# Optimization experiments

Hardware: AMD Instinct MI355X
Metric: run time of the kernel (lower is better)

## Reference

```python
import jax, jax.numpy as jnp
import numpy as np

B, HW, NTGT, C = 2, 4096, 4096, 512
H, KNN = 8, 32
DH = C // H
SCALE = DH ** -0.5


def setup_inputs() -> dict:
    key = jax.random.key(0)
    ks = jax.random.split(key, 12)
    s = 1.0 / np.sqrt(C)
    return {
        "src": jax.random.normal(ks[0], (B, HW, C), jnp.float32),
        "tgt": jax.random.normal(ks[1], (B, NTGT, C), jnp.float32),
        "indices": jax.random.randint(ks[2], (B, HW, KNN), 0, NTGT, jnp.int64),
        "weights": jax.random.normal(ks[3], (B, HW, KNN), jnp.float32),
        "Wq": jax.random.normal(ks[4], (C, C), jnp.float32) * s,
        "bq": jnp.zeros((C,), jnp.float32),
        "Wk": jax.random.normal(ks[5], (C, C), jnp.float32) * s,
        "bk": jnp.zeros((C,), jnp.float32),
        "Wv": jax.random.normal(ks[6], (C, C), jnp.float32) * s,
        "bv": jnp.zeros((C,), jnp.float32),
        "Wo": jax.random.normal(ks[7], (C, C), jnp.float32) * s,
        "bo": jnp.zeros((C,), jnp.float32),
    }


def reference(src, tgt, indices, weights, Wq, bq, Wk, bk, Wv, bv, Wo, bo):
    b, hw, c = src.shape
    # projections -> (b, H, seq, dh)
    q = (src @ Wq + bq).reshape(b, hw, H, DH).transpose(0, 2, 1, 3)
    k = (tgt @ Wk + bk).reshape(b, -1, H, DH).transpose(0, 2, 1, 3)
    v = (tgt @ Wv + bv).reshape(b, -1, H, DH).transpose(0, 2, 1, 3)
    # gather epipolar neighbors: per batch, kb[:, idx] -> (H, hw, KNN, dh)
    gather = jax.vmap(lambda xb, ib: xb[:, ib])
    k_g = gather(k, indices)  # (b, H, hw, KNN, dh)
    v_g = gather(v, indices)  # (b, H, hw, KNN, dh)
    logits = jnp.einsum("bhqd,bhqkd->bhqk", q, k_g) * SCALE
    logits = logits + weights[:, None]  # broadcast over heads
    attn = jax.nn.softmax(logits, axis=-1)
    out = jnp.einsum("bhqk,bhqkd->bhqd", attn, v_g)
    out = out.transpose(0, 2, 1, 3).reshape(b, hw, c)
    return out @ Wo + bo
```

## Files before the change

kernel.cpp:

```cpp
#include <hip/hip_runtime.h>
#include <hip/hip_bf16.h>
#include <stdint.h>
#include <type_traits>

#define B_    2
#define HW_   4096
#define NTGT_ 4096
#define C_    512
#define H_    8
#define KNN_  32
#define DH_   64
#define M_    (B_ * HW_)

typedef unsigned short ushort_t;
typedef __bf16 bf16x8 __attribute__((ext_vector_type(8)));
typedef float floatx4 __attribute__((ext_vector_type(4)));

__device__ __forceinline__ float b2f(ushort_t u) {
    union { uint32_t i; float f; } x;
    x.i = ((uint32_t)u) << 16;
    return x.f;
}
__device__ __forceinline__ ushort_t f2b(float f) {
    union { float f; uint32_t i; } x;
    x.f = f;
    uint32_t r = x.i + 0x7fffu + ((x.i >> 16) & 1u);
    return (ushort_t)(r >> 16);
}
__device__ __forceinline__ uint32_t pk2(float x, float y) {
    union { __hip_bfloat162 h2; uint32_t u; } c;
    c.h2 = __float22bfloat162_rn(make_float2(x, y));
    return c.u;
}
__device__ __forceinline__ uint4 pack8(const float4& a, const float4& b) {
    return make_uint4(pk2(a.x, a.y), pk2(a.z, a.w), pk2(b.x, b.y), pk2(b.z, b.w));
}

__global__ __launch_bounds__(256) void transpose_inplace4_f32(
    float* W0, float* W1, float* W2, float* W3) {
    __shared__ float ta[32][33];
    __shared__ float tb[32][33];

    float* W = (blockIdx.y == 0) ? W0 : (blockIdx.y == 1) ? W1
               : (blockIdx.y == 2) ? W2 : W3;

    int p = blockIdx.x;
    int i = 0, acc = 0;
    while (acc + (16 - i) <= p) { acc += 16 - i; ++i; }
    const int j = i + (p - acc);

    const int t = threadIdx.x;
    const int r = t >> 3;
    const int c0 = (t & 7) * 4;

    {
        float4 d = *(const float4*)&W[(size_t)(i * 32 + r) * 512 + j * 32 + c0];
        ta[r][c0 + 0] = d.x; ta[r][c0 + 1] = d.y;
        ta[r][c0 + 2] = d.z; ta[r][c0 + 3] = d.w;
    }
    if (i != j) {
        float4 d = *(const float4*)&W[(size_t)(j * 32 + r) * 512 + i * 32 + c0];
        tb[r][c0 + 0] = d.x; tb[r][c0 + 1] = d.y;
        tb[r][c0 + 2] = d.z; tb[r][c0 + 3] = d.w;
    }
    __syncthreads();

    *(float4*)&W[(size_t)(j * 32 + r) * 512 + i * 32 + c0] =
        make_float4(ta[c0 + 0][r], ta[c0 + 1][r], ta[c0 + 2][r], ta[c0 + 3][r]);
    if (i != j)
        *(float4*)&W[(size_t)(i * 32 + r) * 512 + j * 32 + c0] =
            make_float4(tb[c0 + 0][r], tb[c0 + 1][r], tb[c0 + 2][r], tb[c0 + 3][r]);
}

template <typename AT, typename OT>
__device__ __forceinline__ void gemm_body(const AT* __restrict__ A,
                                          const float* __restrict__ Wt,
                                          const float* __restrict__ bias,
                                          OT* __restrict__ O,
                                          int bm, int bn) {
    __shared__ ushort_t As[128][40];
    __shared__ ushort_t Bs[64][40];

    const int t = threadIdx.x;
    const int ar = t >> 1;
    const int ak = (t & 1) * 16;
    const int br = t >> 2;
    const int bk = (t & 3) * 8;

    const int lane = t & 63;
    const int wv = t >> 6;
    const int wr = (wv >> 1) * 64;
    const int wc = (wv & 1) * 32;
    const int r16 = lane & 15;
    const int quad = lane >> 4;

    floatx4 acc[4][2] = {};

    for (int kt = 0; kt < 512; kt += 32) {
        uint4 av0, av1, bv0;
        if constexpr (std::is_same<AT, float>::value) {
            const float* p = &A[(size_t)(bm + ar) * 512 + kt + ak];
            av0 = pack8(*(const float4*)p, *(const float4*)(p + 4));
            av1 = pack8(*(const float4*)(p + 8), *(const float4*)(p + 12));
        } else {
            const ushort_t* p = &A[(size_t)(bm + ar) * 512 + kt + ak];
            av0 = *(const uint4*)p;
            av1 = *(const uint4*)(p + 8);
        }
        {
            const float* p = &Wt[(size_t)(bn + br) * 512 + kt + bk];
            bv0 = pack8(*(const float4*)p, *(const float4*)(p + 4));
        }
        __syncthreads();
        *(uint4*)&As[ar][ak] = av0;
        *(uint4*)&As[ar][ak + 8] = av1;
        *(uint4*)&Bs[br][bk] = bv0;
        __syncthreads();

        bf16x8 af[4], bf[2];
#pragma unroll
        for (int i = 0; i < 4; ++i)
            af[i] = *(const bf16x8*)&As[wr + i * 16 + r16][quad * 8];
#pragma unroll
        for (int j = 0; j < 2; ++j)
            bf[j] = *(const bf16x8*)&Bs[wc + j * 16 + r16][quad * 8];
#pragma unroll
        for (int i = 0; i < 4; ++i)
#pragma unroll
            for (int j = 0; j < 2; ++j)
                acc[i][j] = __builtin_amdgcn_mfma_f32_16x16x32_bf16(
                    af[i], bf[j], acc[i][j], 0, 0, 0);
    }

#pragma unroll
    for (int j = 0; j < 2; ++j) {
        const int col = bn + wc + j * 16 + r16;
        const float bj = bias[col];
#pragma unroll
        for (int i = 0; i < 4; ++i) {
            const int row = bm + wr + i * 16 + quad * 4;
#pragma unroll
            for (int r = 0; r < 4; ++r) {
                float v = acc[i][j][r] + bj;
                if constexpr (std::is_same<OT, ushort_t>::value)
                    O[(size_t)(row + r) * 512 + col] = f2b(v);
                else
                    O[(size_t)(row + r) * 512 + col] = v;
            }
        }
    }
}

__global__ __launch_bounds__(256, 4) void gemm_qkv(
    const float* __restrict__ src, const float* __restrict__ tgt,
    const float* __restrict__ WtQ, const float* __restrict__ WtK,
    const float* __restrict__ WtV,
    const float* __restrict__ bq, const float* __restrict__ bk,
    const float* __restrict__ bv,
    ushort_t* __restrict__ Qb, ushort_t* __restrict__ Kb,
    ushort_t* __restrict__ Vb) {
    const int z = blockIdx.z;
    const float* A = (z == 0) ? src : tgt;
    const float* Wt = (z == 0) ? WtQ : (z == 1) ? WtK : WtV;
    const float* bias = (z == 0) ? bq : (z == 1) ? bk : bv;
    ushort_t* O = (z == 0) ? Qb : (z == 1) ? Kb : Vb;
    gemm_body<float, ushort_t>(A, Wt, bias, O, blockIdx.y * 128, blockIdx.x * 64);
}

template <typename OT>
__global__ __launch_bounds__(256, 4) void gemm_o(const ushort_t* __restrict__ A,
                                                 const float* __restrict__ Wt,
                                                 const float* __restrict__ bias,
                                                 OT* __restrict__ O) {
    gemm_body<ushort_t, OT>(A, Wt, bias, O, blockIdx.y * 128, blockIdx.x * 64);
}

#define KVSTRIDE 520
template <typename IT>
__global__ __launch_bounds__(256) void attn_kernel(const ushort_t* Q,
                                                   const ushort_t* __restrict__ K,
                                                   const ushort_t* __restrict__ V,
                                                   const IT* __restrict__ idx,
                                                   const float* __restrict__ wts,
                                                   ushort_t* O) {
    __shared__ float qs[512];
    __shared__ ushort_t kvs[KNN_][KVSTRIDE];
    __shared__ float ps[H_][KNN_];
    __shared__ int idxs[KNN_];
    __shared__ float ws[KNN_];

    const int t = threadIdx.x;
    const int bq = blockIdx.x;
    const int b = bq >> 12;
    const size_t qoff = (size_t)bq * C_;

    {
        uint32_t d = *(const uint32_t*)(Q + qoff + 2 * t);
        qs[2 * t + 0] = b2f((ushort_t)(d & 0xffffu));
        qs[2 * t + 1] = b2f((ushort_t)(d >> 16));
    }
    if (t < KNN_) {
        idxs[t] = (int)idx[(size_t)bq * KNN_ + t];
        ws[t] = wts[(size_t)bq * KNN_ + t];
    }
    __syncthreads();

    const int sr = t >> 3;
    const int sg = (t & 7) * 8;
    {
        const ushort_t* krow = K + ((size_t)(b * NTGT_ + idxs[sr])) * C_;
#pragma unroll
        for (int j = 0; j < 8; ++j) {
            uint4 v = *(const uint4*)(krow + sg + j * 64);
            *(uint4*)&kvs[sr][sg + j * 64] = v;
        }
    }
    __syncthreads();

    const int h = t >> 5;
    const int n = t & 31;
    const float* qh = qs + h * DH_;
    float dot = 0.f;
#pragma unroll
    for (int j = 0; j < 8; ++j) {
        uint4 kv = *(const uint4*)&kvs[n][h * DH_ + j * 8];
        const int d0 = j * 8;
        dot = fmaf(qh[d0 + 0], b2f((ushort_t)(kv.x & 0xffffu)), dot);
        dot = fmaf(qh[d0 + 1], b2f((ushort_t)(kv.x >> 16)), dot);
        dot = fmaf(qh[d0 + 2], b2f((ushort_t)(kv.y & 0xffffu)), dot);
        dot = fmaf(qh[d0 + 3], b2f((ushort_t)(kv.y >> 16)), dot);
        dot = fmaf(qh[d0 + 4], b2f((ushort_t)(kv.z & 0xffffu)), dot);
        dot = fmaf(qh[d0 + 5], b2f((ushort_t)(kv.z >> 16)), dot);
        dot = fmaf(qh[d0 + 6], b2f((ushort_t)(kv.w & 0xffffu)), dot);
        dot = fmaf(qh[d0 + 7], b2f((ushort_t)(kv.w >> 16)), dot);
    }
    float logit = dot * 0.125f + ws[n];

    float mx = logit;
#pragma unroll
    for (int o = 16; o > 0; o >>= 1) mx = fmaxf(mx, __shfl_xor(mx, o));
    float e = __expf(logit - mx);
    float s = e;
#pragma unroll
    for (int o = 16; o > 0; o >>= 1) s += __shfl_xor(s, o);
    ps[h][n] = e / s;
    __syncthreads();

    {
        const ushort_t* vrow = V + ((size_t)(b * NTGT_ + idxs[sr])) * C_;
#pragma unroll
        for (int j = 0; j < 8; ++j) {
            uint4 v = *(const uint4*)(vrow + sg + j * 64);
            *(uint4*)&kvs[sr][sg + j * 64] = v;
        }
    }
    __syncthreads();

    const int d2 = (t & 31) * 2;
    float a0 = 0.f, a1 = 0.f;
#pragma unroll 8
    for (int nn = 0; nn < KNN_; ++nn) {
        uint32_t vv = *(const uint32_t*)&kvs[nn][h * DH_ + d2];
        float p = ps[h][nn];
        a0 = fmaf(p, b2f((ushort_t)(vv & 0xffffu)), a0);
        a1 = fmaf(p, b2f((ushort_t)(vv >> 16)), a1);
    }
    *(uint32_t*)(O + qoff + h * DH_ + d2) = pk2(a0, a1);
}

static int elem_bytes(const void* p, size_t n, int dflt) {
    size_t sz = 0;
    hipError_t err = hipPointerGetAttribute(
        &sz, HIP_POINTER_ATTRIBUTE_RANGE_SIZE, (hipDeviceptr_t)(uintptr_t)p);
    if (err == hipSuccess && sz >= n && (sz % n) == 0) {
        size_t b = sz / n;
        if (b == 2 || b == 4 || b == 8) return (int)b;
    }
    return dflt;
}

extern "C" void kernel_launch(void* const* d_in, const int* in_sizes, int n_in,
                              void* d_out, int out_size, void* d_ws, size_t ws_size,
                              hipStream_t stream) {
    const float* src  = (const float*)d_in[0];
    const float* tgt  = (const float*)d_in[1];
    const void*  idxp = d_in[2];
    const float* wtp  = (const float*)d_in[3];
    float* Wq = (float*)d_in[4];  const float* bq = (const float*)d_in[5];
    float* Wk = (float*)d_in[6];  const float* bk = (const float*)d_in[7];
    float* Wv = (float*)d_in[8];  const float* bv = (const float*)d_in[9];
    float* Wo = (float*)d_in[10]; const float* bo = (const float*)d_in[11];

    const size_t NELEM = (size_t)M_ * C_;
    const size_t NIDX  = (size_t)B_ * HW_ * KNN_;

    const int ib = elem_bytes(idxp, NIDX, 4);
    const int ob = elem_bytes(d_out, NELEM, 4);

    dim3 blk(256);
    dim3 ga(B_ * HW_);

    ushort_t* Qb = (ushort_t*)d_ws;
    ushort_t* Kb = Qb + NELEM;
    ushort_t* Vb = (ushort_t*)d_out;
    ushort_t* Ob = Qb;

    transpose_inplace4_f32<<<dim3(136, 4), blk, 0, stream>>>(Wq, Wk, Wv, Wo);

    gemm_qkv<<<dim3(8, 64, 3), blk, 0, stream>>>(
        src, tgt, Wq, Wk, Wv, bq, bk, bv, Qb, Kb, Vb);

    if (ib == 8)
        attn_kernel<long long><<<ga, blk, 0, stream>>>(
            Qb, Kb, Vb, (const long long*)idxp, wtp, Ob);
    else
        attn_kernel<int><<<ga, blk, 0, stream>>>(
            Qb, Kb, Vb, (const int*)idxp, wtp, Ob);

    if (ob == 2)
        gemm_o<ushort_t><<<dim3(8, 64), blk, 0, stream>>>(
            Ob, Wo, bo, (ushort_t*)d_out);
    else
        gemm_o<float><<<dim3(8, 64), blk, 0, stream>>>(
            Ob, Wo, bo, (float*)d_out);
}
```

Measured before the change: 222.1 us.

## Remap block IDs for XCD-aware L2 locality and coalesce GEMM A loads

Replaces the 2D/3D grids of the QKV and output GEMMs and the attention kernel with 1D grids. Each block ID is decoded so that blocks dispatched round-robin to the same XCD share an M-tile range (GEMMs) or one batch quarter of queries (attention). The goal is better L2 reuse of A rows and of the gathered K/V rows within each XCD's private L2. The GEMM A-tile load is also changed so 4 threads cover a 32-wide row segment and each thread loads two rows 64 apart, matching the B-load pattern. The mapping assumes round-robin dispatch of workgroups across 8 XCDs, which is hardware-specific.

Result: faster. 192.7 us (-13.3%).

```diff
diff --git a/kernel.cpp b/kernel.cpp
--- a/kernel.cpp
+++ b/kernel.cpp
@@ -82,10 +82,8 @@
     __shared__ ushort_t Bs[64][40];
 
     const int t = threadIdx.x;
-    const int ar = t >> 1;
-    const int ak = (t & 1) * 16;
-    const int br = t >> 2;
-    const int bk = (t & 3) * 8;
+    const int lr = t >> 2;
+    const int lc = (t & 3) * 8;
 
     const int lane = t & 63;
     const int wv = t >> 6;
@@ -99,22 +97,22 @@
     for (int kt = 0; kt < 512; kt += 32) {
         uint4 av0, av1, bv0;
         if constexpr (std::is_same<AT, float>::value) {
-            const float* p = &A[(size_t)(bm + ar) * 512 + kt + ak];
-            av0 = pack8(*(const float4*)p, *(const float4*)(p + 4));
-            av1 = pack8(*(const float4*)(p + 8), *(const float4*)(p + 12));
+            const float* p0 = &A[(size_t)(bm + lr) * 512 + kt + lc];
+            const float* p1 = &A[(size_t)(bm + lr + 64) * 512 + kt + lc];
+            av0 = pack8(*(const float4*)p0, *(const float4*)(p0 + 4));
+            av1 = pack8(*(const float4*)p1, *(const float4*)(p1 + 4));
         } else {
-            const ushort_t* p = &A[(size_t)(bm + ar) * 512 + kt + ak];
-            av0 = *(const uint4*)p;
-            av1 = *(const uint4*)(p + 8);
+            av0 = *(const uint4*)&A[(size_t)(bm + lr) * 512 + kt + lc];
+            av1 = *(const uint4*)&A[(size_t)(bm + lr + 64) * 512 + kt + lc];
         }
         {
-            const float* p = &Wt[(size_t)(bn + br) * 512 + kt + bk];
+            const float* p = &Wt[(size_t)(bn + lr) * 512 + kt + lc];
             bv0 = pack8(*(const float4*)p, *(const float4*)(p + 4));
         }
         __syncthreads();
-        *(uint4*)&As[ar][ak] = av0;
-        *(uint4*)&As[ar][ak + 8] = av1;
-        *(uint4*)&Bs[br][bk] = bv0;
+        *(uint4*)&As[lr][lc] = av0;
+        *(uint4*)&As[lr + 64][lc] = av1;
+        *(uint4*)&Bs[lr][lc] = bv0;
         __syncthreads();
 
         bf16x8 af[4], bf[2];
@@ -159,12 +157,20 @@
     const float* __restrict__ bv,
     ushort_t* __restrict__ Qb, ushort_t* __restrict__ Kb,
     ushort_t* __restrict__ Vb) {
-    const int z = blockIdx.z;
+    const int id = blockIdx.x;
+    const int xcd = id & 7;
+    const int g = id >> 3;
+    const int mgrp = g / 24;
+    const int r = g % 24;
+    const int z = r >> 3;
+    const int bn = (r & 7) * 64;
+    const int bm = (xcd + 8 * mgrp) * 128;
+
     const float* A = (z == 0) ? src : tgt;
     const float* Wt = (z == 0) ? WtQ : (z == 1) ? WtK : WtV;
     const float* bias = (z == 0) ? bq : (z == 1) ? bk : bv;
     ushort_t* O = (z == 0) ? Qb : (z == 1) ? Kb : Vb;
-    gemm_body<float, ushort_t>(A, Wt, bias, O, blockIdx.y * 128, blockIdx.x * 64);
+    gemm_body<float, ushort_t>(A, Wt, bias, O, bm, bn);
 }
 
 template <typename OT>
@@ -172,7 +178,13 @@
                                                  const float* __restrict__ Wt,
                                                  const float* __restrict__ bias,
                                                  OT* __restrict__ O) {
-    gemm_body<ushort_t, OT>(A, Wt, bias, O, blockIdx.y * 128, blockIdx.x * 64);
+    const int id = blockIdx.x;
+    const int xcd = id & 7;
+    const int g = id >> 3;
+    const int mgrp = g >> 3;
+    const int bn = (g & 7) * 64;
+    const int bm = (xcd + 8 * mgrp) * 128;
+    gemm_body<ushort_t, OT>(A, Wt, bias, O, bm, bn);
 }
 
 #define KVSTRIDE 520
@@ -190,8 +202,11 @@
     __shared__ float ws[KNN_];
 
     const int t = threadIdx.x;
-    const int bq = blockIdx.x;
-    const int b = bq >> 12;
+    const int id = blockIdx.x;
+    const int xcd = id & 7;
+    const int slot = id >> 3;
+    const int b = xcd >> 2;
+    const int bq = b * HW_ + (xcd & 3) * 1024 + slot;
     const size_t qoff = (size_t)bq * C_;
 
     {
@@ -210,10 +225,8 @@
     {
         const ushort_t* krow = K + ((size_t)(b * NTGT_ + idxs[sr])) * C_;
 #pragma unroll
-        for (int j = 0; j < 8; ++j) {
-            uint4 v = *(const uint4*)(krow + sg + j * 64);
-            *(uint4*)&kvs[sr][sg + j * 64] = v;
-        }
+        for (int j = 0; j < 8; ++j)
+            *(uint4*)&kvs[sr][sg + j * 64] = *(const uint4*)(krow + sg + j * 64);
     }
     __syncthreads();
 
@@ -249,10 +262,8 @@
     {
         const ushort_t* vrow = V + ((size_t)(b * NTGT_ + idxs[sr])) * C_;
 #pragma unroll
-        for (int j = 0; j < 8; ++j) {
-            uint4 v = *(const uint4*)(vrow + sg + j * 64);
-            *(uint4*)&kvs[sr][sg + j * 64] = v;
-        }
+        for (int j = 0; j < 8; ++j)
+            *(uint4*)&kvs[sr][sg + j * 64] = *(const uint4*)(vrow + sg + j * 64);
     }
     __syncthreads();
 
@@ -298,7 +309,6 @@
     const int ob = elem_bytes(d_out, NELEM, 4);
 
     dim3 blk(256);
-    dim3 ga(B_ * HW_);
 
     ushort_t* Qb = (ushort_t*)d_ws;
     ushort_t* Kb = Qb + NELEM;
@@ -307,20 +317,20 @@
 
     transpose_inplace4_f32<<<dim3(136, 4), blk, 0, stream>>>(Wq, Wk, Wv, Wo);
 
-    gemm_qkv<<<dim3(8, 64, 3), blk, 0, stream>>>(
+    gemm_qkv<<<dim3(1536), blk, 0, stream>>>(
         src, tgt, Wq, Wk, Wv, bq, bk, bv, Qb, Kb, Vb);
 
     if (ib == 8)
-        attn_kernel<long long><<<ga, blk, 0, stream>>>(
+        attn_kernel<long long><<<dim3(B_ * HW_), blk, 0, stream>>>(
             Qb, Kb, Vb, (const long long*)idxp, wtp, Ob);
     else
-        attn_kernel<int><<<ga, blk, 0, stream>>>(
+        attn_kernel<int><<<dim3(B_ * HW_), blk, 0, stream>>>(
             Qb, Kb, Vb, (const int*)idxp, wtp, Ob);
 
     if (ob == 2)
-        gemm_o<ushort_t><<<dim3(8, 64), blk, 0, stream>>>(
+        gemm_o<ushort_t><<<dim3(512), blk, 0, stream>>>(
             Ob, Wo, bo, (ushort_t*)d_out);
     else
-        gemm_o<float><<<dim3(8, 64), blk, 0, stream>>>(
+        gemm_o<float><<<dim3(512), blk, 0, stream>>>(
             Ob, Wo, bo, (float*)d_out);
 }
```
